# Optimization experiments

Measured on AMD Instinct MI355X. Metric: run time of the kernel, lower is better.

Reference implementation:

```python
import jax, jax.numpy as jnp
import numpy as np

B, S, E, H = 4, 4096, 1024, 16
D = E // H  # head_dim = 64
EPS = 1e-6


def setup_inputs() -> dict:
    key = jax.random.key(0)
    ks = jax.random.split(key, 11)
    inv = 1.0 / np.sqrt(E)
    return {
        "query": jax.random.normal(ks[0], (B, S, E), dtype=jnp.float32),
        "key": jax.random.normal(ks[1], (B, S, E), dtype=jnp.float32),
        "value": jax.random.normal(ks[2], (B, S, E), dtype=jnp.float32),
        "key_padding_mask": jnp.zeros((B, S), dtype=bool),
        "Wq": jax.random.uniform(ks[3], (E, E), jnp.float32, -inv, inv),
        "bq": jnp.zeros((E,), jnp.float32),
        "Wk": jax.random.uniform(ks[4], (E, E), jnp.float32, -inv, inv),
        "bk": jnp.zeros((E,), jnp.float32),
        "Wv": jax.random.uniform(ks[5], (E, E), jnp.float32, -inv, inv),
        "bv": jnp.zeros((E,), jnp.float32),
        "Wo": jax.random.uniform(ks[6], (E, E), jnp.float32, -inv, inv),
        "bo": jnp.zeros((E,), jnp.float32),
    }


def _heads(x):
    # (B,S,E) -> (B,H,S,D)
    return x.reshape(B, -1, H, D).transpose(0, 2, 1, 3)


def reference(query, key, value, key_padding_mask, Wq, bq, Wk, bk, Wv, bv, Wo, bo):
    q = _heads(query @ Wq.T + bq)
    k = _heads(key @ Wk.T + bk)
    v = _heads(value @ Wv.T + bv)

    q_aug = jax.nn.relu(q) + EPS
    k_aug = jax.nn.relu(k) + EPS
    # mask out padded keys: (B,S_k) -> (B,1,S_k,1)
    k_aug = jnp.where(key_padding_mask[:, None, :, None], 0.0, k_aug)

    kv_context = jnp.einsum("bhsd,bhsv->bhdv", k_aug, v)  # (B,H,D,D)
    k_sum = k_aug.sum(axis=2)                                # (B,H,D)
    denom = jnp.einsum("bhqd,bhd->bhq", q_aug, k_sum)
    denom = jnp.maximum(denom, EPS)

    attn = jnp.einsum("bhqd,bhdv->bhqv", q_aug, kv_context) / denom[..., None]
    attn = attn.transpose(0, 2, 1, 3).reshape(B, -1, E)      # (B,S_q,E)
    # dropout is identity in eval mode
    return attn @ Wo.T + bo
```

## Files before the change

kernel.cpp:

```cpp
#include <hip/hip_runtime.h>
#include <hip/hip_bf16.h>
#include <stdint.h>

#define B_ 4
#define S_ 4096
#define E_ 1024
#define H_ 16
#define D_ 64
#define M_ (B_*S_)
constexpr float kEPS = 1e-6f;

typedef unsigned short u16;
typedef unsigned char  u8;
typedef __bf16 bf16x8 __attribute__((ext_vector_type(8)));
typedef float  f32x4  __attribute__((ext_vector_type(4)));
typedef float  f32x2  __attribute__((ext_vector_type(2)));
typedef u16    u16x8  __attribute__((ext_vector_type(8)));

typedef const __attribute__((address_space(1))) void* gaddr_t;
typedef __attribute__((address_space(3))) void*       laddr_t;

__device__ __forceinline__ u16 f2bf(float f) {
    union { float f; uint32_t u; } v; v.f = f;
    uint32_t u = v.u;
    u += 0x7fffu + ((u >> 16) & 1u);
    return (u16)(u >> 16);
}
__device__ __forceinline__ float bf2f(u16 h) {
    union { uint32_t u; float f; } v; v.u = ((uint32_t)h) << 16;
    return v.f;
}
__device__ __forceinline__ float hi2f(uint32_t d) {
    union { uint32_t u; float f; } v; v.u = d & 0xffff0000u;
    return v.f;
}
__device__ __forceinline__ float lo2f(uint32_t d) {
    union { uint32_t u; float f; } v; v.u = d << 16;
    return v.f;
}

#define VM_WAIT(n) asm volatile("s_waitcnt vmcnt(" #n ")" ::: "memory")
#define LG0        asm volatile("s_waitcnt lgkmcnt(0)" ::: "memory")
#define SBAR       asm volatile("s_barrier" ::: "memory")

__global__ void cvt_kernel(const float* __restrict__ in, u16* __restrict__ out, int n4) {
    int i = blockIdx.x * blockDim.x + threadIdx.x;
    if (i >= n4) return;
    float4 v = reinterpret_cast<const float4*>(in)[i];
    ushort4 o;
    o.x = f2bf(v.x); o.y = f2bf(v.y); o.z = f2bf(v.z); o.w = f2bf(v.w);
    reinterpret_cast<ushort4*>(out)[i] = o;
}

#define BM 256
#define BN 256
#define BKT 64
#define NKT (E_/BKT)

template<int EPI>
__global__ __launch_bounds__(512, 2)
void gemm8(const u16* __restrict__ A, const u16* __restrict__ Bw,
           const float* __restrict__ bias, const u8* __restrict__ mask,
           float* __restrict__ Cf, u16* __restrict__ Cb)
{
    extern __shared__ u16 lds[];
    const int tid  = threadIdx.x;
    const int wid  = tid >> 6, lane = tid & 63;
    const int wqr  = wid >> 2, wqc = wid & 3;
    const int m0   = blockIdx.x * BM;
    const int n0   = blockIdx.y * BN;
    const int fr   = lane & 15;
    const int cg   = lane >> 4;

    const int srow = tid >> 3;
    const int ssc  = tid & 7;
    const int sck  = ssc ^ (srow & 7);
    const u16* aS = A  + (size_t)(m0 + srow)*E_ + sck*8;
    const u16* bS = Bw + (size_t)(n0 + srow)*E_ + sck*8;
    const int sd0 = tid*8, sd1 = (tid + 512)*8;

    int arow[4], brow[2];
#pragma unroll
    for (int mf = 0; mf < 4; ++mf) arow[mf] = (wqr*64 + mf*16 + fr) * 64;
#pragma unroll
    for (int nf = 0; nf < 2; ++nf) brow[nf] = (wqc*32 + nf*16 + fr) * 64;
    const int kx0 = ((cg)     ^ (fr & 7)) * 8;
    const int kx1 = ((4 + cg) ^ (fr & 7)) * 8;

    f32x4 acc[2][2][4][2] = {};
    bf16x8 afr[4][2];

    float bias_v[2][2];
#pragma unroll
    for (int nh = 0; nh < 2; ++nh)
#pragma unroll
        for (int nf = 0; nf < 2; ++nf)
            bias_v[nh][nf] = bias[n0 + nh*128 + wqc*32 + nf*16 + fr];

#define STAGE(BUF, MAT, H, T) do { \
        u16* dst_ = lds + (BUF)*32768 + (MAT)*16384 + (H)*8192; \
        const u16* src_ = ((MAT) ? bS : aS) + (size_t)(H)*128*E_ + (size_t)(T)*BKT; \
        __builtin_amdgcn_global_load_lds((gaddr_t)(src_),                  (laddr_t)(dst_ + sd0), 16, 0, 0); \
        __builtin_amdgcn_global_load_lds((gaddr_t)(src_ + (size_t)64*E_), (laddr_t)(dst_ + sd1), 16, 0, 0); \
    } while (0)

#define PH(BUF, MH, NH, STG_STMT, WAIT_STMT) do { \
        const u16* Ab_ = lds + (BUF)*32768 + (MH)*8192; \
        const u16* Bb_ = lds + (BUF)*32768 + 16384 + (NH)*8192; \
        if ((NH) == 0) { \
            _Pragma("unroll") \
            for (int mf_ = 0; mf_ < 4; ++mf_) { \
                afr[mf_][0] = *reinterpret_cast<const bf16x8*>(Ab_ + arow[mf_] + kx0); \
                afr[mf_][1] = *reinterpret_cast<const bf16x8*>(Ab_ + arow[mf_] + kx1); \
            } \
        } \
        bf16x8 bfv[2][2]; \
        _Pragma("unroll") \
        for (int nf_ = 0; nf_ < 2; ++nf_) { \
            bfv[nf_][0] = *reinterpret_cast<const bf16x8*>(Bb_ + brow[nf_] + kx0); \
            bfv[nf_][1] = *reinterpret_cast<const bf16x8*>(Bb_ + brow[nf_] + kx1); \
        } \
        STG_STMT; \
        WAIT_STMT; \
        SBAR; \
        LG0; \
        __builtin_amdgcn_sched_barrier(0); \
        __builtin_amdgcn_s_setprio(1); \
        _Pragma("unroll") \
        for (int mf_ = 0; mf_ < 4; ++mf_) { \
            _Pragma("unroll") \
            for (int nf_ = 0; nf_ < 2; ++nf_) { \
                acc[MH][NH][mf_][nf_] = __builtin_amdgcn_mfma_f32_16x16x32_bf16(afr[mf_][0], bfv[nf_][0], acc[MH][NH][mf_][nf_], 0, 0, 0); \
                acc[MH][NH][mf_][nf_] = __builtin_amdgcn_mfma_f32_16x16x32_bf16(afr[mf_][1], bfv[nf_][1], acc[MH][NH][mf_][nf_], 0, 0, 0); \
            } \
        } \
        __builtin_amdgcn_s_setprio(0); \
        SBAR; \
    } while (0)

    STAGE(0, 0, 0, 0);
    STAGE(0, 1, 0, 0);
    STAGE(0, 0, 1, 0);
    STAGE(0, 1, 1, 0);
    STAGE(1, 0, 0, 1);
    STAGE(1, 1, 0, 1);
    VM_WAIT(4);
    SBAR;
    __builtin_amdgcn_sched_barrier(0);

#pragma unroll 1
    for (int i = 0; i < 7; ++i) {
        const int T1 = 2*i + 1, T2 = 2*i + 2, T3 = 2*i + 3;
        PH(0, 0, 0, STAGE(1, 0, 1, T1), ;);
        PH(0, 0, 1, STAGE(1, 1, 1, T1), ;);
        PH(0, 1, 0, STAGE(0, 0, 0, T2), ;);
        PH(0, 1, 1, STAGE(0, 1, 0, T2), VM_WAIT(4));
        PH(1, 0, 0, STAGE(0, 0, 1, T2), ;);
        PH(1, 0, 1, STAGE(0, 1, 1, T2), ;);
        PH(1, 1, 0, STAGE(1, 0, 0, T3), ;);
        PH(1, 1, 1, STAGE(1, 1, 0, T3), VM_WAIT(4));
    }
    PH(0, 0, 0, STAGE(1, 0, 1, 15), ;);
    PH(0, 0, 1, STAGE(1, 1, 1, 15), ;);
    PH(0, 1, 0, ;, ;);
    PH(0, 1, 1, ;, VM_WAIT(0));
    PH(1, 0, 0, ;, ;);
    PH(1, 0, 1, ;, ;);
    PH(1, 1, 0, ;, ;);
    PH(1, 1, 1, ;, ;);
#undef PH
#undef STAGE

#pragma unroll
    for (int mh = 0; mh < 2; ++mh) {
#pragma unroll
    for (int nh = 0; nh < 2; ++nh) {
#pragma unroll
    for (int mf = 0; mf < 4; ++mf) {
#pragma unroll
        for (int nf = 0; nf < 2; ++nf) {
            const int gn = n0 + nh*128 + wqc*32 + nf*16 + fr;
#pragma unroll
            for (int r = 0; r < 4; ++r) {
                const int gm = m0 + mh*128 + wqr*64 + mf*16 + cg*4 + r;
                float x = acc[mh][nh][mf][nf][r] + bias_v[nh][nf];
                if (EPI == 0) {
                    Cf[(size_t)gm*E_ + gn] = x;
                } else if (EPI == 1) {
                    x = fmaxf(x, 0.f) + kEPS;
                    Cb[(size_t)gm*E_ + gn] = f2bf(x);
                } else if (EPI == 2) {
                    x = fmaxf(x, 0.f) + kEPS;
                    if (mask[gm]) x = 0.f;
                    Cb[(size_t)gm*E_ + gn] = f2bf(x);
                } else {
                    Cb[(size_t)gm*E_ + gn] = f2bf(x);
                }
            }
        }
    }
    }
    }
}

#define KVS 128
#define KVCH (S_/KVS)
#define KPF 66
__global__ __launch_bounds__(256)
void kv_partial_kernel(const u16* __restrict__ Ka, const u16* __restrict__ Vv,
                       float* __restrict__ kvp, float* __restrict__ ksp)
{
    __shared__ float Ksf[KVS*KPF];
    __shared__ float Vsf[KVS*KPF];
    const int bh = blockIdx.x, b = bh >> 4, h = bh & 15;
    const int s0 = blockIdx.y * KVS;
    const int tid = threadIdx.x;

#pragma unroll
    for (int i = 0; i < 4; ++i) {
        int g = i*256 + tid;
        int row = g >> 3, c8 = (g & 7) * 8;
        size_t goff = (size_t)(b*S_ + s0 + row)*E_ + h*64 + c8;
        bf16x8 kk = *reinterpret_cast<const bf16x8*>(Ka + goff);
        bf16x8 vv = *reinterpret_cast<const bf16x8*>(Vv + goff);
        f32x4 k0, k1, v0, v1;
#pragma unroll
        for (int j = 0; j < 4; ++j) {
            k0[j] = (float)kk[j]; k1[j] = (float)kk[4+j];
            v0[j] = (float)vv[j]; v1[j] = (float)vv[4+j];
        }
        *reinterpret_cast<f32x4*>(Ksf + row*KPF + c8)     = k0;
        *reinterpret_cast<f32x4*>(Ksf + row*KPF + c8 + 4) = k1;
        *reinterpret_cast<f32x4*>(Vsf + row*KPF + c8)     = v0;
        *reinterpret_cast<f32x4*>(Vsf + row*KPF + c8 + 4) = v1;
    }
    __syncthreads();

    const int dg = tid >> 4;
    const int vg = tid & 15;
    f32x2 acc2[4][2] = {};
#pragma unroll 4
    for (int s = 0; s < KVS; ++s) {
        f32x4 k4 = *reinterpret_cast<const f32x4*>(Ksf + s*KPF + dg*4);
        f32x4 v4 = *reinterpret_cast<const f32x4*>(Vsf + s*KPF + vg*4);
        f32x2 va; va[0] = v4[0]; va[1] = v4[1];
        f32x2 vb; vb[0] = v4[2]; vb[1] = v4[3];
#pragma unroll
        for (int d = 0; d < 4; ++d) {
            f32x2 kd; kd[0] = k4[d]; kd[1] = k4[d];
            acc2[d][0] += kd * va;
            acc2[d][1] += kd * vb;
        }
    }
    float* dst = kvp + ((size_t)blockIdx.y*64 + bh)*4096;
#pragma unroll
    for (int d = 0; d < 4; ++d) {
        f32x4 o; o[0] = acc2[d][0][0]; o[1] = acc2[d][0][1]; o[2] = acc2[d][1][0]; o[3] = acc2[d][1][1];
        *reinterpret_cast<f32x4*>(dst + (dg*4 + d)*64 + vg*4) = o;
    }

    __syncthreads();
    {
        const int col = tid & 63, grp = tid >> 6;
        float s = 0.f;
#pragma unroll 8
        for (int r = 0; r < KVS/4; ++r) s += Ksf[(grp*(KVS/4) + r)*KPF + col];
        Vsf[grp*64 + col] = s;
    }
    __syncthreads();
    if (tid < 64) {
        ksp[((size_t)blockIdx.y*64 + bh)*64 + tid] =
            Vsf[tid] + Vsf[64+tid] + Vsf[128+tid] + Vsf[192+tid];
    }
}

__global__ __launch_bounds__(256)
void kv_reduce_kernel(const float* __restrict__ kvp, const float* __restrict__ ksp,
                      u16* __restrict__ kvT, float* __restrict__ ksum)
{
    __shared__ float Tt[16][68];
    const int bh = blockIdx.x >> 2, q = blockIdx.x & 3;
    const int tid = threadIdx.x;

    const size_t base = (size_t)bh*4096 + q*1024 + tid*4;
    f32x4 s = {};
#pragma unroll 8
    for (int c = 0; c < KVCH; ++c) {
        f32x4 x = *reinterpret_cast<const f32x4*>(kvp + (size_t)c*64*4096 + base);
        s[0] += x[0]; s[1] += x[1]; s[2] += x[2]; s[3] += x[3];
    }
    const int dq = tid >> 4, v0 = (tid & 15) * 4;
    Tt[dq][v0] = s[0]; Tt[dq][v0+1] = s[1]; Tt[dq][v0+2] = s[2]; Tt[dq][v0+3] = s[3];

    if (q == 0 && tid < 64) {
        float t = 0.f;
#pragma unroll 8
        for (int c = 0; c < KVCH; ++c) t += ksp[((size_t)c*64 + bh)*64 + tid];
        ksum[bh*64 + tid] = t;
    }
    __syncthreads();

    if (tid < 64) {
        const int v = tid;
        u16x8 o0, o1;
#pragma unroll
        for (int j = 0; j < 8; ++j) { o0[j] = f2bf(Tt[j][v]); o1[j] = f2bf(Tt[8+j][v]); }
        u16* dst = kvT + (size_t)bh*4096 + v*64 + q*16;
        *reinterpret_cast<u16x8*>(dst)     = o0;
        *reinterpret_cast<u16x8*>(dst + 8) = o1;
    }
}

__global__ __launch_bounds__(256)
void attn_kernel(const u16* __restrict__ Qa, const u16* __restrict__ kvT,
                 const float* __restrict__ ksum, u16* __restrict__ attn)
{
    __shared__ u16  Qs[256*64];
    __shared__ u16  Ts[64*64];
    __shared__ float kss[64];
    __shared__ float invd[256];

    const int bh = blockIdx.x, b = bh >> 4, h = bh & 15;
    const int s0 = blockIdx.y * 256;
    const int tid = threadIdx.x;
    const int wid = tid >> 6, lane = tid & 63;
    const int fr = lane & 15, cg = lane >> 4;

#pragma unroll
    for (int j = 0; j < 8; ++j) {
        int L = (wid*8 + j)*64 + lane;
        int row = L >> 3, c = L & 7;
        int cs = c ^ (row & 7);
        const u16* src = Qa + (size_t)(b*S_ + s0 + row)*E_ + h*64 + cs*8;
        __builtin_amdgcn_global_load_lds((gaddr_t)src, (laddr_t)(Qs + L*8), 16, 0, 0);
    }
#pragma unroll
    for (int k = 0; k < 2; ++k) {
        int g = k*256 + tid;
        int v = g >> 3, c = g & 7;
        uint4 q = *reinterpret_cast<const uint4*>(kvT + (size_t)bh*4096 + g*8);
        int cs = c ^ (v & 7);
        *reinterpret_cast<uint4*>(Ts + v*64 + cs*8) = q;
    }
    if (tid < 64) kss[tid] = ksum[bh*64 + tid];
    asm volatile("s_waitcnt vmcnt(0) lgkmcnt(0)" ::: "memory");
    __syncthreads();

    {
        float den = 0.f;
#pragma unroll
        for (int c = 0; c < 8; ++c) {
            uint4 qc = *reinterpret_cast<const uint4*>(Qs + tid*64 + (c ^ (tid & 7))*8);
            den += lo2f(qc.x)*kss[c*8+0] + hi2f(qc.x)*kss[c*8+1]
                 + lo2f(qc.y)*kss[c*8+2] + hi2f(qc.y)*kss[c*8+3]
                 + lo2f(qc.z)*kss[c*8+4] + hi2f(qc.z)*kss[c*8+5]
                 + lo2f(qc.w)*kss[c*8+6] + hi2f(qc.w)*kss[c*8+7];
        }
        invd[tid] = 1.0f / fmaxf(den, kEPS);
    }
    __syncthreads();

    f32x4 acc[4][4] = {};
#pragma unroll
    for (int ks = 0; ks < 2; ++ks) {
        bf16x8 bfrag[4];
#pragma unroll
        for (int nf = 0; nf < 4; ++nf) {
            int v = nf*16 + fr;
            bfrag[nf] = *reinterpret_cast<const bf16x8*>(Ts + v*64 + ((ks*4 + cg) ^ (v & 7))*8);
        }
#pragma unroll
        for (int mf = 0; mf < 4; ++mf) {
            int m = wid*64 + mf*16 + fr;
            bf16x8 afrag = *reinterpret_cast<const bf16x8*>(Qs + m*64 + ((ks*4 + cg) ^ (m & 7))*8);
#pragma unroll
            for (int nf = 0; nf < 4; ++nf)
                acc[mf][nf] = __builtin_amdgcn_mfma_f32_16x16x32_bf16(afrag, bfrag[nf], acc[mf][nf], 0, 0, 0);
        }
    }

#pragma unroll
    for (int mf = 0; mf < 4; ++mf) {
#pragma unroll
        for (int nf = 0; nf < 4; ++nf) {
            const int v = nf*16 + fr;
#pragma unroll
            for (int r = 0; r < 4; ++r) {
                const int row = wid*64 + mf*16 + cg*4 + r;
                float x = acc[mf][nf][r] * invd[row];
                attn[(size_t)(b*S_ + s0 + row)*E_ + h*64 + v] = f2bf(x);
            }
        }
    }
}

extern "C" void kernel_launch(void* const* d_in, const int* in_sizes, int n_in,
                              void* d_out, int out_size, void* d_ws, size_t ws_size,
                              hipStream_t stream)
{
    const float* query = (const float*)d_in[0];
    const float* key   = (const float*)d_in[1];
    const float* value = (const float*)d_in[2];
    const u8*    mask  = (const u8*)d_in[3];
    const float* Wq = (const float*)d_in[4];
    const float* bq = (const float*)d_in[5];
    const float* Wk = (const float*)d_in[6];
    const float* bk = (const float*)d_in[7];
    const float* Wv = (const float*)d_in[8];
    const float* bv = (const float*)d_in[9];
    const float* Wo = (const float*)d_in[10];
    const float* bo = (const float*)d_in[11];
    float* out = (float*)d_out;

    const size_t SZ_ME = (size_t)M_ * E_;
    const size_t SZ_EE = (size_t)E_ * E_;

    char* ws = (char*)d_ws;
    u16* qx   = (u16*)ws; ws += SZ_ME*2;
    u16* kx   = (u16*)ws; ws += SZ_ME*2;
    u16* vx   = (u16*)ws; ws += SZ_ME*2;
    u16* Qa   = (u16*)ws; ws += SZ_ME*2;
    u16* Ka   = (u16*)ws; ws += SZ_ME*2;
    u16* Vv   = (u16*)ws; ws += SZ_ME*2;
    u16* wqb  = (u16*)ws; ws += SZ_EE*2;
    u16* wkb  = (u16*)ws; ws += SZ_EE*2;
    u16* wvb  = (u16*)ws; ws += SZ_EE*2;
    u16* wob  = (u16*)ws; ws += SZ_EE*2;

    u16*   attnb = qx;
    float* kvp   = (float*)kx;
    float* ksp   = (float*)vx;
    u16*   kvT   = (u16*)((char*)vx + (size_t)KVCH*64*64*4);
    float* ksum  = (float*)((char*)kvT + (size_t)64*4096*2);

    cvt_kernel<<<(int)(SZ_ME/4/256), 256, 0, stream>>>(query, qx, (int)(SZ_ME/4));
    cvt_kernel<<<(int)(SZ_ME/4/256), 256, 0, stream>>>(key,   kx, (int)(SZ_ME/4));
    cvt_kernel<<<(int)(SZ_ME/4/256), 256, 0, stream>>>(value, vx, (int)(SZ_ME/4));
    cvt_kernel<<<(int)(SZ_EE/4/256), 256, 0, stream>>>(Wq, wqb, (int)(SZ_EE/4));
    cvt_kernel<<<(int)(SZ_EE/4/256), 256, 0, stream>>>(Wk, wkb, (int)(SZ_EE/4));
    cvt_kernel<<<(int)(SZ_EE/4/256), 256, 0, stream>>>(Wv, wvb, (int)(SZ_EE/4));
    cvt_kernel<<<(int)(SZ_EE/4/256), 256, 0, stream>>>(Wo, wob, (int)(SZ_EE/4));

    dim3 ggrid(M_/BM, E_/BN);
    constexpr size_t LDS_BYTES = 2 * 32768 * sizeof(u16);
    gemm8<1><<<ggrid, 512, LDS_BYTES, stream>>>(qx, wqb, bq, nullptr, nullptr, Qa);
    gemm8<2><<<ggrid, 512, LDS_BYTES, stream>>>(kx, wkb, bk, mask,    nullptr, Ka);
    gemm8<3><<<ggrid, 512, LDS_BYTES, stream>>>(vx, wvb, bv, nullptr, nullptr, Vv);

    kv_partial_kernel<<<dim3(B_*H_, KVCH), 256, 0, stream>>>(Ka, Vv, kvp, ksp);
    kv_reduce_kernel<<<256, 256, 0, stream>>>(kvp, ksp, kvT, ksum);

    attn_kernel<<<dim3(B_*H_, S_/256), 256, 0, stream>>>(Qa, kvT, ksum, attnb);

    gemm8<0><<<ggrid, 512, LDS_BYTES, stream>>>(attnb, wob, bo, nullptr, out, nullptr);
}
```

Measured before the change: 284.1 us.

## Store K/V projections transposed and compute KV context with MFMA

The K and V projection GEMM epilogues now write their outputs transposed (per batch, feature-major with sequence contiguous) using 4-element vector stores. This lets a new kv kernel compute K^T·V per head with bf16 MFMA instructions, reading straight from global memory, instead of converting to fp32 in LDS and doing scalar FMAs. The sequence split drops from 32 chunks to 8, which shrinks the partial buffer and lets the reduce kernel become a flat elementwise sum. The risks are strided, less coalesced transposed stores in the GEMM epilogue and fewer blocks in the kv stage.

```diff
diff --git a/kernel.cpp b/kernel.cpp
--- a/kernel.cpp
+++ b/kernel.cpp
@@ -14,7 +14,6 @@
 typedef unsigned char  u8;
 typedef __bf16 bf16x8 __attribute__((ext_vector_type(8)));
 typedef float  f32x4  __attribute__((ext_vector_type(4)));
-typedef float  f32x2  __attribute__((ext_vector_type(2)));
 typedef u16    u16x8  __attribute__((ext_vector_type(8)));
 
 typedef const __attribute__((address_space(1))) void* gaddr_t;
@@ -25,10 +24,6 @@
     uint32_t u = v.u;
     u += 0x7fffu + ((u >> 16) & 1u);
     return (u16)(u >> 16);
-}
-__device__ __forceinline__ float bf2f(u16 h) {
-    union { uint32_t u; float f; } v; v.u = ((uint32_t)h) << 16;
-    return v.f;
 }
 __device__ __forceinline__ float hi2f(uint32_t d) {
     union { uint32_t u; float f; } v; v.u = d & 0xffff0000u;
@@ -171,6 +166,8 @@
 #undef PH
 #undef STAGE
 
+    const int bblk = m0 >> 12;
+    const int sloc = m0 & 4095;
 #pragma unroll
     for (int mh = 0; mh < 2; ++mh) {
 #pragma unroll
@@ -180,21 +177,30 @@
 #pragma unroll
         for (int nf = 0; nf < 2; ++nf) {
             const int gn = n0 + nh*128 + wqc*32 + nf*16 + fr;
-#pragma unroll
-            for (int r = 0; r < 4; ++r) {
-                const int gm = m0 + mh*128 + wqr*64 + mf*16 + cg*4 + r;
-                float x = acc[mh][nh][mf][nf][r] + bias_v[nh][nf];
-                if (EPI == 0) {
-                    Cf[(size_t)gm*E_ + gn] = x;
-                } else if (EPI == 1) {
-                    x = fmaxf(x, 0.f) + kEPS;
-                    Cb[(size_t)gm*E_ + gn] = f2bf(x);
-                } else if (EPI == 2) {
-                    x = fmaxf(x, 0.f) + kEPS;
-                    if (mask[gm]) x = 0.f;
-                    Cb[(size_t)gm*E_ + gn] = f2bf(x);
-                } else {
-                    Cb[(size_t)gm*E_ + gn] = f2bf(x);
+            const int mb = mh*128 + wqr*64 + mf*16 + cg*4;
+            if (EPI == 2 || EPI == 3) {
+                ushort4 o;
+#pragma unroll
+                for (int r = 0; r < 4; ++r) {
+                    float x = acc[mh][nh][mf][nf][r] + bias_v[nh][nf];
+                    if (EPI == 2) {
+                        x = fmaxf(x, 0.f) + kEPS;
+                        if (mask[m0 + mb + r]) x = 0.f;
+                    }
+                    ((u16*)&o)[r] = f2bf(x);
+                }
+                *reinterpret_cast<ushort4*>(Cb + ((size_t)(bblk*1024 + gn))*4096 + sloc + mb) = o;
+            } else {
+#pragma unroll
+                for (int r = 0; r < 4; ++r) {
+                    const int gm = m0 + mb + r;
+                    float x = acc[mh][nh][mf][nf][r] + bias_v[nh][nf];
+                    if (EPI == 0) {
+                        Cf[(size_t)gm*E_ + gn] = x;
+                    } else {
+                        x = fmaxf(x, 0.f) + kEPS;
+                        Cb[(size_t)gm*E_ + gn] = f2bf(x);
+                    }
                 }
             }
         }
@@ -203,111 +209,70 @@
     }
 }
 
-#define KVS 128
-#define KVCH (S_/KVS)
-#define KPF 66
+#define NSC 8
+#define KCH (S_/NSC)
 __global__ __launch_bounds__(256)
-void kv_partial_kernel(const u16* __restrict__ Ka, const u16* __restrict__ Vv,
-                       float* __restrict__ kvp, float* __restrict__ ksp)
+void kv_mfma_kernel(const u16* __restrict__ KaT, const u16* __restrict__ VvT,
+                    float* __restrict__ kvp, float* __restrict__ ksp)
 {
-    __shared__ float Ksf[KVS*KPF];
-    __shared__ float Vsf[KVS*KPF];
-    const int bh = blockIdx.x, b = bh >> 4, h = bh & 15;
-    const int s0 = blockIdx.y * KVS;
+    __shared__ float sm[4][64];
+    const int bh = blockIdx.x, sc = blockIdx.y;
     const int tid = threadIdx.x;
-
-#pragma unroll
-    for (int i = 0; i < 4; ++i) {
-        int g = i*256 + tid;
-        int row = g >> 3, c8 = (g & 7) * 8;
-        size_t goff = (size_t)(b*S_ + s0 + row)*E_ + h*64 + c8;
-        bf16x8 kk = *reinterpret_cast<const bf16x8*>(Ka + goff);
-        bf16x8 vv = *reinterpret_cast<const bf16x8*>(Vv + goff);
-        f32x4 k0, k1, v0, v1;
-#pragma unroll
-        for (int j = 0; j < 4; ++j) {
-            k0[j] = (float)kk[j]; k1[j] = (float)kk[4+j];
-            v0[j] = (float)vv[j]; v1[j] = (float)vv[4+j];
-        }
-        *reinterpret_cast<f32x4*>(Ksf + row*KPF + c8)     = k0;
-        *reinterpret_cast<f32x4*>(Ksf + row*KPF + c8 + 4) = k1;
-        *reinterpret_cast<f32x4*>(Vsf + row*KPF + c8)     = v0;
-        *reinterpret_cast<f32x4*>(Vsf + row*KPF + c8 + 4) = v1;
+    const int w = tid >> 6, lane = tid & 63;
+    const int fr = lane & 15, cg = lane >> 4;
+
+    const u16* Ar = VvT + ((size_t)bh*64 + w*16 + fr)*4096 + sc*KCH;
+    const u16* Br0 = KaT + ((size_t)bh*64 + fr)*4096 + sc*KCH;
+
+    f32x4 acc[4] = {};
+#pragma unroll 2
+    for (int ks = 0; ks < KCH/32; ++ks) {
+        const int ko = ks*32 + cg*8;
+        bf16x8 af = *reinterpret_cast<const bf16x8*>(Ar + ko);
+#pragma unroll
+        for (int nf = 0; nf < 4; ++nf) {
+            bf16x8 bf = *reinterpret_cast<const bf16x8*>(Br0 + (size_t)nf*16*4096 + ko);
+            acc[nf] = __builtin_amdgcn_mfma_f32_16x16x32_bf16(af, bf, acc[nf], 0, 0, 0);
+        }
+    }
+    float* dst = kvp + ((size_t)sc*64 + bh)*4096;
+#pragma unroll
+    for (int nf = 0; nf < 4; ++nf)
+#pragma unroll
+        for (int r = 0; r < 4; ++r)
+            dst[(w*16 + cg*4 + r)*64 + nf*16 + fr] = acc[nf][r];
+
+    {
+        const int d = tid & 63, qq = tid >> 6;
+        const u16* kr = KaT + ((size_t)bh*64 + d)*4096 + sc*KCH + qq*(KCH/4);
+        float s = 0.f;
+#pragma unroll 4
+        for (int i = 0; i < KCH/4/8; ++i) {
+            bf16x8 kk = *reinterpret_cast<const bf16x8*>(kr + i*8);
+#pragma unroll
+            for (int j = 0; j < 8; ++j) s += (float)kk[j];
+        }
+        sm[qq][d] = s;
     }
     __syncthreads();
-
-    const int dg = tid >> 4;
-    const int vg = tid & 15;
-    f32x2 acc2[4][2] = {};
-#pragma unroll 4
-    for (int s = 0; s < KVS; ++s) {
-        f32x4 k4 = *reinterpret_cast<const f32x4*>(Ksf + s*KPF + dg*4);
-        f32x4 v4 = *reinterpret_cast<const f32x4*>(Vsf + s*KPF + vg*4);
-        f32x2 va; va[0] = v4[0]; va[1] = v4[1];
-        f32x2 vb; vb[0] = v4[2]; vb[1] = v4[3];
-#pragma unroll
-        for (int d = 0; d < 4; ++d) {
-            f32x2 kd; kd[0] = k4[d]; kd[1] = k4[d];
-            acc2[d][0] += kd * va;
-            acc2[d][1] += kd * vb;
-        }
-    }
-    float* dst = kvp + ((size_t)blockIdx.y*64 + bh)*4096;
-#pragma unroll
-    for (int d = 0; d < 4; ++d) {
-        f32x4 o; o[0] = acc2[d][0][0]; o[1] = acc2[d][0][1]; o[2] = acc2[d][1][0]; o[3] = acc2[d][1][1];
-        *reinterpret_cast<f32x4*>(dst + (dg*4 + d)*64 + vg*4) = o;
-    }
-
-    __syncthreads();
-    {
-        const int col = tid & 63, grp = tid >> 6;
-        float s = 0.f;
-#pragma unroll 8
-        for (int r = 0; r < KVS/4; ++r) s += Ksf[(grp*(KVS/4) + r)*KPF + col];
-        Vsf[grp*64 + col] = s;
-    }
-    __syncthreads();
-    if (tid < 64) {
-        ksp[((size_t)blockIdx.y*64 + bh)*64 + tid] =
-            Vsf[tid] + Vsf[64+tid] + Vsf[128+tid] + Vsf[192+tid];
-    }
+    if (tid < 64)
+        ksp[((size_t)sc*64 + bh)*64 + tid] = sm[0][tid] + sm[1][tid] + sm[2][tid] + sm[3][tid];
 }
 
 __global__ __launch_bounds__(256)
 void kv_reduce_kernel(const float* __restrict__ kvp, const float* __restrict__ ksp,
                       u16* __restrict__ kvT, float* __restrict__ ksum)
 {
-    __shared__ float Tt[16][68];
-    const int bh = blockIdx.x >> 2, q = blockIdx.x & 3;
-    const int tid = threadIdx.x;
-
-    const size_t base = (size_t)bh*4096 + q*1024 + tid*4;
-    f32x4 s = {};
-#pragma unroll 8
-    for (int c = 0; c < KVCH; ++c) {
-        f32x4 x = *reinterpret_cast<const f32x4*>(kvp + (size_t)c*64*4096 + base);
-        s[0] += x[0]; s[1] += x[1]; s[2] += x[2]; s[3] += x[3];
-    }
-    const int dq = tid >> 4, v0 = (tid & 15) * 4;
-    Tt[dq][v0] = s[0]; Tt[dq][v0+1] = s[1]; Tt[dq][v0+2] = s[2]; Tt[dq][v0+3] = s[3];
-
-    if (q == 0 && tid < 64) {
+    const int i = blockIdx.x*256 + threadIdx.x;
+    float s = 0.f;
+#pragma unroll
+    for (int c = 0; c < NSC; ++c) s += kvp[(size_t)c*262144 + i];
+    kvT[i] = f2bf(s);
+    if (i < 4096) {
         float t = 0.f;
-#pragma unroll 8
-        for (int c = 0; c < KVCH; ++c) t += ksp[((size_t)c*64 + bh)*64 + tid];
-        ksum[bh*64 + tid] = t;
-    }
-    __syncthreads();
-
-    if (tid < 64) {
-        const int v = tid;
-        u16x8 o0, o1;
-#pragma unroll
-        for (int j = 0; j < 8; ++j) { o0[j] = f2bf(Tt[j][v]); o1[j] = f2bf(Tt[8+j][v]); }
-        u16* dst = kvT + (size_t)bh*4096 + v*64 + q*16;
-        *reinterpret_cast<u16x8*>(dst)     = o0;
-        *reinterpret_cast<u16x8*>(dst + 8) = o1;
+#pragma unroll
+        for (int c = 0; c < NSC; ++c) t += ksp[(size_t)c*4096 + i];
+        ksum[i] = t;
     }
 }
 
@@ -420,8 +385,8 @@
     u16* kx   = (u16*)ws; ws += SZ_ME*2;
     u16* vx   = (u16*)ws; ws += SZ_ME*2;
     u16* Qa   = (u16*)ws; ws += SZ_ME*2;
-    u16* Ka   = (u16*)ws; ws += SZ_ME*2;
-    u16* Vv   = (u16*)ws; ws += SZ_ME*2;
+    u16* KaT  = (u16*)ws; ws += SZ_ME*2;
+    u16* VvT  = (u16*)ws; ws += SZ_ME*2;
     u16* wqb  = (u16*)ws; ws += SZ_EE*2;
     u16* wkb  = (u16*)ws; ws += SZ_EE*2;
     u16* wvb  = (u16*)ws; ws += SZ_EE*2;
@@ -430,7 +395,7 @@
     u16*   attnb = qx;
     float* kvp   = (float*)kx;
     float* ksp   = (float*)vx;
-    u16*   kvT   = (u16*)((char*)vx + (size_t)KVCH*64*64*4);
+    u16*   kvT   = (u16*)((char*)vx + (size_t)NSC*4096*4);
     float* ksum  = (float*)((char*)kvT + (size_t)64*4096*2);
 
     cvt_kernel<<<(int)(SZ_ME/4/256), 256, 0, stream>>>(query, qx, (int)(SZ_ME/4));
@@ -444,11 +409,11 @@
     dim3 ggrid(M_/BM, E_/BN);
     constexpr size_t LDS_BYTES = 2 * 32768 * sizeof(u16);
     gemm8<1><<<ggrid, 512, LDS_BYTES, stream>>>(qx, wqb, bq, nullptr, nullptr, Qa);
-    gemm8<2><<<ggrid, 512, LDS_BYTES, stream>>>(kx, wkb, bk, mask,    nullptr, Ka);
-    gemm8<3><<<ggrid, 512, LDS_BYTES, stream>>>(vx, wvb, bv, nullptr, nullptr, Vv);
-
-    kv_partial_kernel<<<dim3(B_*H_, KVCH), 256, 0, stream>>>(Ka, Vv, kvp, ksp);
-    kv_reduce_kernel<<<256, 256, 0, stream>>>(kvp, ksp, kvT, ksum);
+    gemm8<2><<<ggrid, 512, LDS_BYTES, stream>>>(kx, wkb, bk, mask,    nullptr, KaT);
+    gemm8<3><<<ggrid, 512, LDS_BYTES, stream>>>(vx, wvb, bv, nullptr, nullptr, VvT);
+
+    kv_mfma_kernel<<<dim3(64, NSC), 256, 0, stream>>>(KaT, VvT, kvp, ksp);
+    kv_reduce_kernel<<<1024, 256, 0, stream>>>(kvp, ksp, kvT, ksum);
 
     attn_kernel<<<dim3(B_*H_, S_/256), 256, 0, stream>>>(Qa, kvT, ksum, attnb);
 
```

Result: faster. 266.7 us (-6.1%).
